# Kernel tuning notes

Measured on AMD Instinct MI355X. Metric: run time of the kernel, lower is better.

The kernel has to match this reference:

```python
import jax, jax.numpy as jnp
import numpy as np

D = 768
B, T = 4, 4096


def _layernorm(x, gamma, bias):
    # Faithful to the (buggy) original: (x - mu/sqrt(var)) * gamma + bias,
    # with torch's default unbiased variance (ddof=1).
    mu = jnp.mean(x, axis=-1, keepdims=True)
    var = jnp.var(x, axis=-1, keepdims=True, ddof=1)
    return (x - mu / jnp.sqrt(var)) * gamma + bias


def setup_inputs() -> dict:
    key = jax.random.key(0)
    ks = jax.random.split(key, 8)
    # kaiming_uniform_ default: bound = sqrt(6 / fan_in) with a=sqrt(5) -> gain = sqrt(2/(1+5)) = sqrt(1/3)
    # bound = gain * sqrt(3/fan_in) = sqrt(1/fan_in)
    bound_attn = 1.0 / np.sqrt(D)
    bound_lin = 1.0 / np.sqrt(D)  # torch Linear default init bound
    return {
        "x": jax.random.normal(ks[0], (B, T, D), dtype=jnp.float32),
        "ln1_g": jnp.ones((D,), jnp.float32),
        "ln1_b": jnp.zeros((D,), jnp.float32),
        "wq": jax.random.uniform(ks[1], (D, D), jnp.float32, -bound_attn, bound_attn),
        "wk": jax.random.uniform(ks[2], (D, D), jnp.float32, -bound_attn, bound_attn),
        "wv": jax.random.uniform(ks[3], (D, D), jnp.float32, -bound_attn, bound_attn),
        "ln2_g": jnp.ones((D,), jnp.float32),
        "ln2_b": jnp.zeros((D,), jnp.float32),
        "fc1_w": jax.random.uniform(ks[4], (D, D), jnp.float32, -bound_lin, bound_lin),
        "fc1_b": jax.random.uniform(ks[5], (D,), jnp.float32, -bound_lin, bound_lin),
        "fc2_w": jax.random.uniform(ks[6], (D, D), jnp.float32, -bound_lin, bound_lin),
        "fc2_b": jax.random.uniform(ks[7], (D,), jnp.float32, -bound_lin, bound_lin),
    }


def reference(x, ln1_g, ln1_b, wq, wk, wv, ln2_g, ln2_b, fc1_w, fc1_b, fc2_w, fc2_b):
    d_model = x.shape[-1]
    # LN 1
    y = _layernorm(x, ln1_g, ln1_b)
    # Naive single-head attention (no causal mask, scale 1/sqrt(d_model))
    q = jnp.einsum("btk,kd->btd", y, wq)
    k = jnp.einsum("btk,kd->btd", y, wk)
    v = jnp.einsum("btk,kd->btd", y, wv)
    scale = 1.0 / jnp.sqrt(jnp.asarray(d_model, y.dtype))
    a = jax.nn.softmax(jnp.einsum("bqd,bkd->bqk", q, k) * scale, axis=-1)
    y = jnp.einsum("bqt,btd->bqd", a, v)
    # LN 2
    y = _layernorm(y, ln2_g, ln2_b)
    # MLP: Linear -> ReLU -> Linear (Dropout in eval mode = identity)
    h = jax.nn.relu(jnp.einsum("btd,od->bto", y, fc1_w) + fc1_b)
    y = jnp.einsum("btd,od->bto", h, fc2_w) + fc2_b
    # Residual
    return x + y
```

## Files before the change

### kernel.cpp

```cpp
#include <hip/hip_runtime.h>
#include <hip/hip_bf16.h>
#include <hip/hip_fp8.h>


#define DDIM 768
#define TT   4096
#define NB   4
#define ROWS (NB * TT)
#define CTS  136

using bf16 = __hip_bfloat16;
typedef __bf16 bf16x8 __attribute__((ext_vector_type(8)));
typedef float  f32x4  __attribute__((ext_vector_type(4)));

__device__ __forceinline__ float to_f(float x) { return x; }
__device__ __forceinline__ float to_f(bf16 x) { return __bfloat162float(x); }

__device__ __forceinline__ unsigned char to_fp8(float f) {
  __hip_fp8_e4m3 t(f);
  return (unsigned char)t.__x;
}

__device__ __forceinline__ void gload16(const void* g, void* l) {
#if __has_builtin(__builtin_amdgcn_global_load_lds)
  __builtin_amdgcn_global_load_lds(
      (const __attribute__((address_space(1))) void*)g,
      (__attribute__((address_space(3))) void*)l, 16, 0, 0);
#else
  int lane = threadIdx.x & 63;
  ((int4*)l)[lane] = *(const int4*)g;
#endif
}

template <int MODE, int NT, int MT>
__global__ __launch_bounds__(256) void gemm_bt(
    const bf16* __restrict__ A, int lda, long sA,
    const bf16* __restrict__ B, int ldb, long sB,
    void* __restrict__ Cout, int ldc, long sC, int K, float scale,
    const float* __restrict__ bias, const float* __restrict__ resid,
    float* __restrict__ Lsum) {
  constexpr int SMEMN = (MODE == 4) ? 8192 : (128 * CTS);
  __shared__ __align__(16) bf16 smem[SMEMN];
  __shared__ float Lred[128];
  bf16* As = smem;
  bf16* Bs = smem + 4096;

  int bx, by, bz;
  if constexpr (NT > 0) {
    const int h   = blockIdx.x;
    const int xcd = h & 7;
    const int s   = h >> 3;
    bx = s % NT;
    const int group = (s / NT) * 8 + xcd;
    by = group % MT;
    bz = group / MT;
  } else {
    bx = blockIdx.x; by = blockIdx.y; bz = blockIdx.z;
  }

  A += (long)bz * sA;
  B += (long)bz * sB;

  const int tid  = threadIdx.x;
  const int wave = tid >> 6;
  const int lane = tid & 63;
  const int l16  = lane & 15;
  const int lq   = lane >> 4;
  const int wm   = wave >> 1;
  const int wn   = wave & 1;
  const long tileM = (long)by * 128;
  const long tileN = (long)bx * 128;

  if constexpr (MODE == 5) {
    if (tid < 128) Lred[tid] = 0.f;
  }

  f32x4 acc[4][4] = {};

  const int c0 = wave * 128 + lane;
  const int c1 = c0 + 64;
  bf16* ldsA0 = &As[(wave * 128 + 0) * 8];
  bf16* ldsA1 = &As[(wave * 128 + 64) * 8];
  bf16* ldsB0 = &Bs[(wave * 128 + 0) * 8];
  bf16* ldsB1 = &Bs[(wave * 128 + 64) * 8];
  const long ar0 = (tileM + (c0 >> 2)) * (long)lda + (c0 & 3) * 8;
  const long ar1 = (tileM + (c1 >> 2)) * (long)lda + (c1 & 3) * 8;
  const long br0 = (tileN + (c0 >> 2)) * (long)ldb + (c0 & 3) * 8;
  const long br1 = (tileN + (c1 >> 2)) * (long)ldb + (c1 & 3) * 8;

  for (int k0 = 0; k0 < K; k0 += 32) {
    gload16(A + ar0 + k0, ldsA0);
    gload16(A + ar1 + k0, ldsA1);
    gload16(B + br0 + k0, ldsB0);
    gload16(B + br1 + k0, ldsB1);
    __syncthreads();

    bf16x8 af[4], bf_[4];
#pragma unroll
    for (int i = 0; i < 4; ++i)
      af[i] = *(const bf16x8*)&As[(wm * 64 + i * 16 + l16) * 32 + lq * 8];
#pragma unroll
    for (int j = 0; j < 4; ++j)
      bf_[j] = *(const bf16x8*)&Bs[(wn * 64 + j * 16 + l16) * 32 + lq * 8];
#pragma unroll
    for (int i = 0; i < 4; ++i)
#pragma unroll
      for (int j = 0; j < 4; ++j)
        acc[i][j] = __builtin_amdgcn_mfma_f32_16x16x32_bf16(af[i], bf_[j],
                                                            acc[i][j], 0, 0, 0);
    __syncthreads();
  }

  if constexpr (MODE == 5) {
    bf16* ctile = smem;
    float ps[4][4] = {};
#pragma unroll
    for (int i = 0; i < 4; ++i)
#pragma unroll
      for (int j = 0; j < 4; ++j)
#pragma unroll
        for (int r = 0; r < 4; ++r) {
          float p = __expf(acc[i][j][r] * scale);
          ctile[(wm * 64 + i * 16 + lq * 4 + r) * CTS + wn * 64 + j * 16 + l16] =
              __float2bfloat16(p);
          ps[i][r] += p;
        }
#pragma unroll
    for (int i = 0; i < 4; ++i)
#pragma unroll
      for (int r = 0; r < 4; ++r) {
        float v = ps[i][r];
        v += __shfl_xor(v, 1);
        v += __shfl_xor(v, 2);
        v += __shfl_xor(v, 4);
        v += __shfl_xor(v, 8);
        if (l16 == 0) atomicAdd(&Lred[wm * 64 + i * 16 + lq * 4 + r], v);
      }
    __syncthreads();
    if (tid < 128) atomicAdd(&Lsum[(long)bz * TT + tileM + tid], Lred[tid]);
    unsigned char* Pz = (unsigned char*)Cout + (long)bz * sC;
#pragma unroll
    for (int p = 0; p < 8; ++p) {
      const int rr = p * 16 + (tid >> 4);
      const int cc = (tid & 15) * 8;
      bf16x8 v = *(bf16x8*)&ctile[rr * CTS + cc];
      union { unsigned char b[8]; uint2 u; } pk;
#pragma unroll
      for (int e = 0; e < 8; ++e) pk.b[e] = to_fp8((float)v[e]);
      *(uint2*)&Pz[(long)(tileM + rr) * ldc + tileN + cc] = pk.u;
    }
  } else if constexpr (MODE == 3) {
    bf16* ctile = smem;
#pragma unroll
    for (int j = 0; j < 4; ++j) {
      const float bj = bias[tileN + wn * 64 + j * 16 + l16];
#pragma unroll
      for (int i = 0; i < 4; ++i)
#pragma unroll
        for (int r = 0; r < 4; ++r) {
          float v = acc[i][j][r] + bj;
          v = v > 0.f ? v : 0.f;
          ctile[(wm * 64 + i * 16 + lq * 4 + r) * CTS + wn * 64 + j * 16 + l16] =
              __float2bfloat16(v);
        }
    }
    __syncthreads();
    bf16* Cb = (bf16*)Cout;
#pragma unroll
    for (int p = 0; p < 8; ++p) {
      const int rr = p * 16 + (tid >> 4);
      const int cc = (tid & 15) * 8;
      float4 v = *(float4*)&ctile[rr * CTS + cc];
      *(float4*)&Cb[(long)(tileM + rr) * ldc + tileN + cc] = v;
    }
  } else {
#pragma unroll
    for (int i = 0; i < 4; ++i)
#pragma unroll
      for (int j = 0; j < 4; ++j)
#pragma unroll
        for (int r = 0; r < 4; ++r) {
          const long row = tileM + wm * 64 + i * 16 + lq * 4 + r;
          const long col = tileN + wn * 64 + j * 16 + l16;
          float v = acc[i][j][r] + bias[col] + resid[row * ldc + col];
          ((float*)Cout)[row * ldc + col] = v;
        }
  }
}

__global__ __launch_bounds__(256) void gemm_pv(
    const unsigned char* __restrict__ P,
    const unsigned char* __restrict__ Vt,
    bf16* __restrict__ O,
    const float* __restrict__ Lsum) {
  __shared__ __align__(16) unsigned char smem8[128 * CTS * 2];
  unsigned char* As8 = smem8;
  unsigned char* Bs8 = smem8 + 4096;
  bf16* ctile = (bf16*)smem8;

  const int h   = blockIdx.x;
  const int xcd = h & 7;
  const int s   = h >> 3;
  const int bx  = s % 6;
  const int grp = (s / 6) * 8 + xcd;
  const int by  = grp % 32;
  const int bz  = grp / 32;

  const int tid  = threadIdx.x;
  const int wave = tid >> 6;
  const int lane = tid & 63;
  const int l16  = lane & 15;
  const int lq   = lane >> 4;
  const int wm   = wave >> 1;
  const int wn   = wave & 1;
  const long tileM = (long)by * 128;
  const long tileN = (long)bx * 128;

  const unsigned char* Pz = P + (long)bz * TT * TT;
  const unsigned char* Vz = Vt + (long)bz * TT;

  f32x4 acc[4][4] = {};

  const int c = wave * 64 + lane;
  const long pa = (tileM + (c >> 1)) * (long)TT + (c & 1) * 16;
  const long va = (tileN + (c >> 1)) * (long)ROWS + (c & 1) * 16;
  unsigned char* ldsA = As8 + wave * 1024;
  unsigned char* ldsB = Bs8 + wave * 1024;

  for (int k0 = 0; k0 < TT; k0 += 32) {
    gload16(Pz + pa + k0, ldsA);
    gload16(Vz + va + k0, ldsB);
    __syncthreads();

    long af[4], bfr[4];
#pragma unroll
    for (int i = 0; i < 4; ++i)
      af[i] = *(const long*)&As8[(wm * 64 + i * 16 + l16) * 32 + lq * 8];
#pragma unroll
    for (int j = 0; j < 4; ++j)
      bfr[j] = *(const long*)&Bs8[(wn * 64 + j * 16 + l16) * 32 + lq * 8];
#pragma unroll
    for (int i = 0; i < 4; ++i)
#pragma unroll
      for (int j = 0; j < 4; ++j)
        acc[i][j] = __builtin_amdgcn_mfma_f32_16x16x32_fp8_fp8(
            af[i], bfr[j], acc[i][j], 0, 0, 0);
    __syncthreads();
  }

  float inv[4][4];
#pragma unroll
  for (int i = 0; i < 4; ++i)
#pragma unroll
    for (int r = 0; r < 4; ++r)
      inv[i][r] =
          1.0f / Lsum[(long)bz * TT + tileM + wm * 64 + i * 16 + lq * 4 + r];
#pragma unroll
  for (int i = 0; i < 4; ++i)
#pragma unroll
    for (int j = 0; j < 4; ++j)
#pragma unroll
      for (int r = 0; r < 4; ++r)
        ctile[(wm * 64 + i * 16 + lq * 4 + r) * CTS + wn * 64 + j * 16 + l16] =
            __float2bfloat16(acc[i][j][r] * inv[i][r]);
  __syncthreads();
#pragma unroll
  for (int p = 0; p < 8; ++p) {
    const int rr = p * 16 + (tid >> 4);
    const int cc = (tid & 15) * 8;
    float4 v = *(float4*)&ctile[rr * CTS + cc];
    *(float4*)&O[((long)bz * TT + tileM + rr) * DDIM + tileN + cc] = v;
  }
}

__global__ __launch_bounds__(256) void gemm_qkv(
    const bf16* __restrict__ A,
    const bf16* __restrict__ Wq, const bf16* __restrict__ Wk,
    const bf16* __restrict__ Wv, bf16* __restrict__ Qm,
    bf16* __restrict__ Km, unsigned char* __restrict__ Vt) {
  __shared__ __align__(16) bf16 smem[128 * CTS];
  bf16* As = smem;
  bf16* Bs = smem + 4096;
  bf16* ctile = smem;

  const int z = blockIdx.z;
  const bf16* B = (z == 0) ? Wq : (z == 1) ? Wk : Wv;

  const int tid  = threadIdx.x;
  const int wave = tid >> 6;
  const int lane = tid & 63;
  const int l16  = lane & 15;
  const int lq   = lane >> 4;
  const int wm   = wave >> 1;
  const int wn   = wave & 1;
  const long tileM = (long)blockIdx.y * 128;
  const long tileN = (long)blockIdx.x * 128;

  f32x4 acc[4][4] = {};

  const int c0 = wave * 128 + lane;
  const int c1 = c0 + 64;
  bf16* ldsA0 = &As[(wave * 128 + 0) * 8];
  bf16* ldsA1 = &As[(wave * 128 + 64) * 8];
  bf16* ldsB0 = &Bs[(wave * 128 + 0) * 8];
  bf16* ldsB1 = &Bs[(wave * 128 + 64) * 8];
  const long ar0 = (tileM + (c0 >> 2)) * (long)DDIM + (c0 & 3) * 8;
  const long ar1 = (tileM + (c1 >> 2)) * (long)DDIM + (c1 & 3) * 8;
  const long br0 = (tileN + (c0 >> 2)) * (long)DDIM + (c0 & 3) * 8;
  const long br1 = (tileN + (c1 >> 2)) * (long)DDIM + (c1 & 3) * 8;

  for (int k0 = 0; k0 < DDIM; k0 += 32) {
    gload16(A + ar0 + k0, ldsA0);
    gload16(A + ar1 + k0, ldsA1);
    gload16(B + br0 + k0, ldsB0);
    gload16(B + br1 + k0, ldsB1);
    __syncthreads();

    bf16x8 af[4], bf_[4];
#pragma unroll
    for (int i = 0; i < 4; ++i)
      af[i] = *(const bf16x8*)&As[(wm * 64 + i * 16 + l16) * 32 + lq * 8];
#pragma unroll
    for (int j = 0; j < 4; ++j)
      bf_[j] = *(const bf16x8*)&Bs[(wn * 64 + j * 16 + l16) * 32 + lq * 8];
#pragma unroll
    for (int i = 0; i < 4; ++i)
#pragma unroll
      for (int j = 0; j < 4; ++j)
        acc[i][j] = __builtin_amdgcn_mfma_f32_16x16x32_bf16(af[i], bf_[j],
                                                            acc[i][j], 0, 0, 0);
    __syncthreads();
  }

  if (z < 2) {
#pragma unroll
    for (int i = 0; i < 4; ++i)
#pragma unroll
      for (int j = 0; j < 4; ++j)
#pragma unroll
        for (int r = 0; r < 4; ++r)
          ctile[(wm * 64 + i * 16 + lq * 4 + r) * CTS + wn * 64 + j * 16 + l16] =
              __float2bfloat16(acc[i][j][r]);
    __syncthreads();
    bf16* Cp = (z == 0) ? Qm : Km;
#pragma unroll
    for (int p = 0; p < 8; ++p) {
      const int rr = p * 16 + (tid >> 4);
      const int cc = (tid & 15) * 8;
      float4 v = *(float4*)&ctile[rr * CTS + cc];
      *(float4*)&Cp[(long)(tileM + rr) * DDIM + tileN + cc] = v;
    }
  } else {
#pragma unroll
    for (int i = 0; i < 4; ++i)
#pragma unroll
      for (int j = 0; j < 4; ++j) {
        union { bf16 h[4]; uint2 u; } w;
#pragma unroll
        for (int r = 0; r < 4; ++r) w.h[r] = __float2bfloat16(acc[i][j][r]);
        *(uint2*)&ctile[(wn * 64 + j * 16 + l16) * CTS + wm * 64 + i * 16 +
                        lq * 4] = w.u;
      }
    __syncthreads();
#pragma unroll
    for (int p = 0; p < 8; ++p) {
      const int rr = p * 16 + (tid >> 4);
      const int cc = (tid & 15) * 8;
      bf16x8 v = *(bf16x8*)&ctile[rr * CTS + cc];
      union { unsigned char b[8]; uint2 u; } pk;
#pragma unroll
      for (int e = 0; e < 8; ++e) pk.b[e] = to_fp8((float)v[e]);
      *(uint2*)&Vt[(long)(tileN + rr) * ROWS + tileM + cc] = pk.u;
    }
  }
}

template <typename T>
__global__ __launch_bounds__(256) void ln_kernel(
    const T* __restrict__ in, const float* __restrict__ g,
    const float* __restrict__ beta, bf16* __restrict__ out,
    float* __restrict__ Lzero) {
  const long row = blockIdx.x;
  if (Lzero != nullptr && threadIdx.x == 0) Lzero[row] = 0.f;
  const T* xr = in + row * DDIM;
  const int t = threadIdx.x;
  float v0 = to_f(xr[t]), v1 = to_f(xr[t + 256]), v2 = to_f(xr[t + 512]);
  float s = v0 + v1 + v2;
  float q = v0 * v0 + v1 * v1 + v2 * v2;
#pragma unroll
  for (int o = 32; o; o >>= 1) {
    s += __shfl_down(s, o);
    q += __shfl_down(q, o);
  }
  __shared__ float sb[4], qb[4];
  if ((t & 63) == 0) { sb[t >> 6] = s; qb[t >> 6] = q; }
  __syncthreads();
  const float S = sb[0] + sb[1] + sb[2] + sb[3];
  const float Q = qb[0] + qb[1] + qb[2] + qb[3];
  const float mu  = S * (1.0f / 768.0f);
  const float var = (Q - 768.0f * mu * mu) * (1.0f / 767.0f);
  const float sub = mu / sqrtf(var);
  bf16* orow = out + row * DDIM;
  orow[t]       = __float2bfloat16((v0 - sub) * g[t]       + beta[t]);
  orow[t + 256] = __float2bfloat16((v1 - sub) * g[t + 256] + beta[t + 256]);
  orow[t + 512] = __float2bfloat16((v2 - sub) * g[t + 512] + beta[t + 512]);
}

__global__ void prep_weights(const float* __restrict__ wq,
                             const float* __restrict__ wk,
                             const float* __restrict__ wv,
                             const float* __restrict__ f1,
                             const float* __restrict__ f2,
                             bf16* wqt, bf16* wkt, bf16* wvt, bf16* f1b,
                             bf16* f2b) {
  __shared__ float tile[32][33];
  const float* src;
  bf16* dst;
  bool tr = true;
  switch (blockIdx.z) {
    case 0: src = wq; dst = wqt; break;
    case 1: src = wk; dst = wkt; break;
    case 2: src = wv; dst = wvt; break;
    case 3: src = f1; dst = f1b; tr = false; break;
    default: src = f2; dst = f2b; tr = false; break;
  }
  const int tx = threadIdx.x, ty = threadIdx.y;
  const int x = blockIdx.x * 32 + tx;
  const int y = blockIdx.y * 32 + ty;
  if (tr) {
#pragma unroll
    for (int r = 0; r < 4; ++r) tile[ty + 8 * r][tx] = src[(y + 8 * r) * DDIM + x];
    __syncthreads();
    const int ox = blockIdx.y * 32 + tx;
    const int oy = blockIdx.x * 32 + ty;
#pragma unroll
    for (int r = 0; r < 4; ++r)
      dst[(oy + 8 * r) * DDIM + ox] = __float2bfloat16(tile[tx][ty + 8 * r]);
  } else {
#pragma unroll
    for (int r = 0; r < 4; ++r)
      dst[(y + 8 * r) * DDIM + x] = __float2bfloat16(src[(y + 8 * r) * DDIM + x]);
  }
}

extern "C" void kernel_launch(void* const* d_in, const int* in_sizes, int n_in,
                              void* d_out, int out_size, void* d_ws,
                              size_t ws_size, hipStream_t stream) {
  const float* x     = (const float*)d_in[0];
  const float* ln1_g = (const float*)d_in[1];
  const float* ln1_b = (const float*)d_in[2];
  const float* wq    = (const float*)d_in[3];
  const float* wk    = (const float*)d_in[4];
  const float* wv    = (const float*)d_in[5];
  const float* ln2_g = (const float*)d_in[6];
  const float* ln2_b = (const float*)d_in[7];
  const float* f1w   = (const float*)d_in[8];
  const float* f1bias= (const float*)d_in[9];
  const float* f2w   = (const float*)d_in[10];
  const float* f2bias= (const float*)d_in[11];
  float* out = (float*)d_out;

  char* ws = (char*)d_ws;
  size_t off = 0;
  auto take = [&](size_t bytes) -> char* {
    char* p = ws + off;
    off += (bytes + 255) & ~(size_t)255;
    return p;
  };
  const size_t WB = (size_t)DDIM * DDIM * sizeof(bf16);
  const size_t MB = (size_t)ROWS * DDIM * sizeof(bf16);
  bf16* wqt = (bf16*)take(WB);
  bf16* wkt = (bf16*)take(WB);
  bf16* wvt = (bf16*)take(WB);
  bf16* f1b = (bf16*)take(WB);
  bf16* f2b = (bf16*)take(WB);
  float* Lsum = (float*)take((size_t)ROWS * sizeof(float));
  bf16* y1  = (bf16*)take(MB);
  bf16* Qm  = (bf16*)take(MB);
  bf16* Km  = (bf16*)take(MB);
  unsigned char* Vt8 = (unsigned char*)take((size_t)DDIM * ROWS);
  unsigned char* Sb8 = (unsigned char*)take((size_t)NB * TT * TT);
  bf16* O  = y1;
  bf16* y2 = Qm;
  bf16* h  = Km;

  prep_weights<<<dim3(24, 24, 5), dim3(32, 8), 0, stream>>>(
      wq, wk, wv, f1w, f2w, wqt, wkt, wvt, f1b, f2b);

  ln_kernel<float><<<ROWS, 256, 0, stream>>>(x, ln1_g, ln1_b, y1, Lsum);

  gemm_qkv<<<dim3(6, 128, 3), 256, 0, stream>>>(y1, wqt, wkt, wvt, Qm, Km, Vt8);

  const float scale = 0.03608439182435161f;
  gemm_bt<5, 32, 32><<<dim3(32 * 32 * NB), 256, 0, stream>>>(
      Qm, DDIM, (long)TT * DDIM, Km, DDIM, (long)TT * DDIM, Sb8, TT,
      (long)TT * TT, DDIM, scale, nullptr, nullptr, Lsum);

  gemm_pv<<<dim3(6 * 32 * NB), 256, 0, stream>>>(Sb8, Vt8, O, Lsum);

  ln_kernel<bf16><<<ROWS, 256, 0, stream>>>(O, ln2_g, ln2_b, y2, nullptr);

  gemm_bt<3, 0, 0><<<dim3(6, 128, 1), 256, 0, stream>>>(
      y2, DDIM, 0, f1b, DDIM, 0, h, DDIM, 0, DDIM, 1.f, f1bias, nullptr,
      nullptr);
  gemm_bt<4, 0, 0><<<dim3(6, 128, 1), 256, 0, stream>>>(
      h, DDIM, 0, f2b, DDIM, 0, out, DDIM, 0, DDIM, 1.f, f2bias, x, nullptr);
}
```

Baseline: 647.4 us.

## Write fp8 score and V tiles directly from registers via swapped operands

The QK^T GEMM now takes K as the A operand and Q as the B operand, so each lane's four accumulator values are contiguous key columns of one query row. Those values are packed with the hardware fp8 convert instruction and stored as 4-byte words straight to global memory. This removes the LDS staging tile, one barrier and the per-element conversions. The V-transpose epilogue gets the same treatment, shared memory for non-MODE-3 variants shrinks, and row sums are reduced over the new lane layout. The cost is narrower, more scattered global stores (4 bytes per lane, strided rows) in place of coalesced 8-byte row writes.

```diff
diff --git a/kernel.cpp b/kernel.cpp
--- a/kernel.cpp
+++ b/kernel.cpp
@@ -16,9 +16,19 @@
 __device__ __forceinline__ float to_f(float x) { return x; }
 __device__ __forceinline__ float to_f(bf16 x) { return __bfloat162float(x); }
 
-__device__ __forceinline__ unsigned char to_fp8(float f) {
-  __hip_fp8_e4m3 t(f);
-  return (unsigned char)t.__x;
+__device__ __forceinline__ int pack_fp8x4(float a, float b, float c, float d) {
+#if __has_builtin(__builtin_amdgcn_cvt_pk_fp8_f32)
+  int w = __builtin_amdgcn_cvt_pk_fp8_f32(a, b, 0, false);
+  w = __builtin_amdgcn_cvt_pk_fp8_f32(c, d, w, true);
+  return w;
+#else
+  union { unsigned char bb[4]; int w; } u;
+  u.bb[0] = (unsigned char)__hip_fp8_e4m3(a).__x;
+  u.bb[1] = (unsigned char)__hip_fp8_e4m3(b).__x;
+  u.bb[2] = (unsigned char)__hip_fp8_e4m3(c).__x;
+  u.bb[3] = (unsigned char)__hip_fp8_e4m3(d).__x;
+  return u.w;
+#endif
 }
 
 __device__ __forceinline__ void gload16(const void* g, void* l) {
@@ -39,7 +49,7 @@
     void* __restrict__ Cout, int ldc, long sC, int K, float scale,
     const float* __restrict__ bias, const float* __restrict__ resid,
     float* __restrict__ Lsum) {
-  constexpr int SMEMN = (MODE == 4) ? 8192 : (128 * CTS);
+  constexpr int SMEMN = (MODE == 3) ? (128 * CTS) : 8192;
   __shared__ __align__(16) bf16 smem[SMEMN];
   __shared__ float Lred[128];
   bf16* As = smem;
@@ -112,43 +122,32 @@
   }
 
   if constexpr (MODE == 5) {
-    bf16* ctile = smem;
-    float ps[4][4] = {};
-#pragma unroll
-    for (int i = 0; i < 4; ++i)
-#pragma unroll
-      for (int j = 0; j < 4; ++j)
-#pragma unroll
-        for (int r = 0; r < 4; ++r) {
-          float p = __expf(acc[i][j][r] * scale);
-          ctile[(wm * 64 + i * 16 + lq * 4 + r) * CTS + wn * 64 + j * 16 + l16] =
-              __float2bfloat16(p);
-          ps[i][r] += p;
-        }
-#pragma unroll
-    for (int i = 0; i < 4; ++i)
-#pragma unroll
-      for (int r = 0; r < 4; ++r) {
-        float v = ps[i][r];
-        v += __shfl_xor(v, 1);
-        v += __shfl_xor(v, 2);
-        v += __shfl_xor(v, 4);
-        v += __shfl_xor(v, 8);
-        if (l16 == 0) atomicAdd(&Lred[wm * 64 + i * 16 + lq * 4 + r], v);
+    unsigned char* Pz = (unsigned char*)Cout + (long)bz * sC;
+    float ps[4] = {0.f, 0.f, 0.f, 0.f};
+#pragma unroll
+    for (int j = 0; j < 4; ++j) {
+      const long qrow = tileN + wn * 64 + j * 16 + l16;
+#pragma unroll
+      for (int i = 0; i < 4; ++i) {
+        const float p0 = __expf(acc[i][j][0] * scale);
+        const float p1 = __expf(acc[i][j][1] * scale);
+        const float p2 = __expf(acc[i][j][2] * scale);
+        const float p3 = __expf(acc[i][j][3] * scale);
+        ps[j] += (p0 + p1) + (p2 + p3);
+        const int w = pack_fp8x4(p0, p1, p2, p3);
+        const long kcol = tileM + wm * 64 + i * 16 + lq * 4;
+        *(int*)&Pz[qrow * (long)ldc + kcol] = w;
       }
-    __syncthreads();
-    if (tid < 128) atomicAdd(&Lsum[(long)bz * TT + tileM + tid], Lred[tid]);
-    unsigned char* Pz = (unsigned char*)Cout + (long)bz * sC;
-#pragma unroll
-    for (int p = 0; p < 8; ++p) {
-      const int rr = p * 16 + (tid >> 4);
-      const int cc = (tid & 15) * 8;
-      bf16x8 v = *(bf16x8*)&ctile[rr * CTS + cc];
-      union { unsigned char b[8]; uint2 u; } pk;
-#pragma unroll
-      for (int e = 0; e < 8; ++e) pk.b[e] = to_fp8((float)v[e]);
-      *(uint2*)&Pz[(long)(tileM + rr) * ldc + tileN + cc] = pk.u;
-    }
+    }
+#pragma unroll
+    for (int j = 0; j < 4; ++j) {
+      float v = ps[j];
+      v += __shfl_xor(v, 16);
+      v += __shfl_xor(v, 32);
+      if (lq == 0) atomicAdd(&Lred[wn * 64 + j * 16 + l16], v);
+    }
+    __syncthreads();
+    if (tid < 128) atomicAdd(&Lsum[(long)bz * TT + tileN + tid], Lred[tid]);
   } else if constexpr (MODE == 3) {
     bf16* ctile = smem;
 #pragma unroll
@@ -352,25 +351,15 @@
     }
   } else {
 #pragma unroll
-    for (int i = 0; i < 4; ++i)
-#pragma unroll
-      for (int j = 0; j < 4; ++j) {
-        union { bf16 h[4]; uint2 u; } w;
-#pragma unroll
-        for (int r = 0; r < 4; ++r) w.h[r] = __float2bfloat16(acc[i][j][r]);
-        *(uint2*)&ctile[(wn * 64 + j * 16 + l16) * CTS + wm * 64 + i * 16 +
-                        lq * 4] = w.u;
+    for (int j = 0; j < 4; ++j) {
+      const long nrow = tileN + wn * 64 + j * 16 + l16;
+#pragma unroll
+      for (int i = 0; i < 4; ++i) {
+        const int w = pack_fp8x4(acc[i][j][0], acc[i][j][1], acc[i][j][2],
+                                 acc[i][j][3]);
+        const long mcol = tileM + wm * 64 + i * 16 + lq * 4;
+        *(int*)&Vt[nrow * (long)ROWS + mcol] = w;
       }
-    __syncthreads();
-#pragma unroll
-    for (int p = 0; p < 8; ++p) {
-      const int rr = p * 16 + (tid >> 4);
-      const int cc = (tid & 15) * 8;
-      bf16x8 v = *(bf16x8*)&ctile[rr * CTS + cc];
-      union { unsigned char b[8]; uint2 u; } pk;
-#pragma unroll
-      for (int e = 0; e < 8; ++e) pk.b[e] = to_fp8((float)v[e]);
-      *(uint2*)&Vt[(long)(tileN + rr) * ROWS + tileM + cc] = pk.u;
     }
   }
 }
@@ -493,7 +482,7 @@
 
   const float scale = 0.03608439182435161f;
   gemm_bt<5, 32, 32><<<dim3(32 * 32 * NB), 256, 0, stream>>>(
-      Qm, DDIM, (long)TT * DDIM, Km, DDIM, (long)TT * DDIM, Sb8, TT,
+      Km, DDIM, (long)TT * DDIM, Qm, DDIM, (long)TT * DDIM, Sb8, TT,
       (long)TT * TT, DDIM, scale, nullptr, nullptr, Lsum);
 
   gemm_pv<<<dim3(6 * 32 * NB), 256, 0, stream>>>(Sb8, Vt8, O, Lsum);
```

New measurement: 646.1 us. About the same (-0.2%).
